# Kernel tuning notes

Hardware: AMD Instinct MI355X
Metric: run time of the kernel (lower is better)

## Reference

```python
import jax, jax.numpy as jnp
import numpy as np

N_NODES = 50000
C = 128
E = 800000
B = 4096
NEG = 5
NUM_LAYERS = 3


def setup_inputs() -> dict:
    key = jax.random.key(0)
    ks = jax.random.split(key, 8)
    edge_index = jax.random.randint(ks[0], (2, E), 0, N_NODES, dtype=jnp.int64)
    edge_weight = jax.random.uniform(ks[1], (E,), dtype=jnp.float32)
    n_id = jax.random.randint(ks[2], ((2 + NEG) * B,), 0, N_NODES, dtype=jnp.int64)
    x = jnp.zeros((1,), jnp.float32)  # ignored by forward (overwritten by id_embed)
    id_embed = jax.random.normal(ks[3], (N_NODES, C), jnp.float32) * 0.1
    w1 = jax.random.normal(ks[4], (2 * C, C), jnp.float32) * (1.0 / np.sqrt(2 * C))
    b1 = jnp.zeros((C,), jnp.float32)
    w2 = jax.random.normal(ks[5], (C, 1), jnp.float32) * (1.0 / np.sqrt(C))
    b2 = jnp.zeros((1,), jnp.float32)
    return {"x": x, "edge_index": edge_index, "edge_weight": edge_weight,
            "n_id": n_id, "neg_sample_num": NEG, "id_embed": id_embed,
            "w1": w1, "b1": b1, "w2": w2, "b2": b2}


def reference(x, edge_index, edge_weight, n_id, neg_sample_num, id_embed, w1, b1, w2, b2):
    n_nodes = id_embed.shape[0]
    row, col = edge_index[0], edge_index[1]
    # symmetric GCN normalization (LGCConv)
    deg = jax.ops.segment_sum(jnp.ones_like(row, dtype=id_embed.dtype), row,
                              num_segments=n_nodes)
    dinv = jnp.where(deg > 0, jax.lax.rsqrt(jnp.maximum(deg, 1e-12)), 0.0)
    norm = (dinv[row] * dinv[col])[:, None]  # [E,1]
    h = id_embed
    final = id_embed
    for _ in range(NUM_LAYERS):
        h = jax.ops.segment_sum(norm * h[col], row, num_segments=n_nodes)
        final = final + h
    final = final / (NUM_LAYERS + 1)
    # split n_id into (out, pos, neg) index groups
    b = n_id.shape[0] // (2 + neg_sample_num)
    out = final[n_id[:b]]
    pos = final[n_id[b:2 * b]]
    neg = final[n_id[2 * b:]]
    tiled_out = jnp.repeat(out, neg_sample_num, axis=0)  # [b*neg, C]

    def pred_head(z):  # Linear -> LeakyReLU(0.2) -> (Dropout eval=identity) -> Linear
        z = jax.nn.leaky_relu(z @ w1 + b1, negative_slope=0.2)
        return z @ w2 + b2

    pos_logit = pred_head(jnp.concatenate([out, pos], axis=-1))
    neg_logits = pred_head(jnp.concatenate([tiled_out, neg], axis=-1))
    return pos_logit, neg_logits
```

## Files before the change

kernel.cpp:

```cpp
#include <hip/hip_runtime.h>
#include <hip/hip_bf16.h>

#define C 128
#define NBKT 128
#define BCAP 8192

typedef __bf16 bf16x8 __attribute__((ext_vector_type(8)));
typedef float floatx4 __attribute__((ext_vector_type(4)));

__device__ __forceinline__ unsigned short f2bf(float f) {
    unsigned u = __float_as_uint(f);
    unsigned r = (u + 0x7FFFu + ((u >> 16) & 1u)) >> 16;
    return (unsigned short)r;
}
__device__ __forceinline__ float bflo(unsigned v) { return __uint_as_float(v << 16); }
__device__ __forceinline__ float bfhi(unsigned v) { return __uint_as_float(v & 0xFFFF0000u); }
__device__ __forceinline__ unsigned packbf(float lo, float hi) {
    return (unsigned)f2bf(lo) | ((unsigned)f2bf(hi) << 16);
}

__device__ __forceinline__ int g_idx(const void* p, long long i, int is64) {
    if (is64) return (int)((const long long*)p)[i];
    return ((const int*)p)[i];
}
__device__ __forceinline__ float g_flt(const void* p, long long i, int isf32) {
    if (isf32) return ((const float*)p)[i];
    return __uint_as_float(((unsigned)((const unsigned short*)p)[i]) << 16);
}

__global__ void k_detect(const void* edge, const void* nid, const void* emb, int* flags,
                         unsigned* g0, unsigned* g1, unsigned* g2, int* bucketcnt,
                         int N, int SST) {
    int t = threadIdx.x;
    int buf = t >> 6, w = t & 63;
    size_t o = (size_t)(w >> 5) * SST + (size_t)N * 32 + (w & 31);
    if (buf == 0) g0[o] = 0;
    else if (buf == 1) g1[o] = 0;
    else g2[o] = 0;
    if (t < NBKT) bucketcnt[t] = 0;
    if (t < 64) {
        const unsigned* wrd = (const unsigned*)edge;
        const unsigned* nw = (const unsigned*)nid;
        int predA = (t < 32) ? (wrd[2 * t + 1] == 0u) : 1;
        int predB = (t < 32) ? (nw[2 * t + 1] == 0u) : 1;
        const unsigned short* h = (const unsigned short*)emb;
        int ex = (h[2 * t] >> 7) & 0xFF;
        int plaus = (ex >= 0x6C && ex <= 0x7F) ? 1 : 0;
        unsigned long long mA = __ballot(predA);
        unsigned long long mB = __ballot(predB);
        unsigned long long mP = __ballot(plaus);
        if (t == 0) {
            flags[0] = (mA == ~0ull) ? 1 : 0;
            flags[1] = (mB == ~0ull) ? 1 : 0;
            flags[2] = (__popcll(mP) < 32) ? 1 : 0;
        }
    }
}

__global__ void k_bucketA(const void* edge, int E, int rpb, const int* flags,
                          unsigned* __restrict__ bucketbuf, int* __restrict__ bucketcnt) {
    __shared__ int lcnt[NBKT];
    __shared__ int lbase[NBKT];
    int t = threadIdx.x;
    int is64 = flags[0];
    const int PER = 8;
    int chunkSz = blockDim.x * PER;
    long long stride = (long long)gridDim.x * chunkSz;
    for (long long base = (long long)blockIdx.x * chunkSz; base < E; base += stride) {
        if (t < NBKT) lcnt[t] = 0;
        __syncthreads();
        int bkt[PER], rank[PER];
        unsigned enc[PER];
        long long e0 = base + (long long)t * PER;
        int rr[PER], cc[PER];
        if (e0 + PER <= E) {
            if (is64) {
                const long long* pr = (const long long*)edge + e0;
                const long long* pc = (const long long*)edge + E + e0;
#pragma unroll
                for (int j = 0; j < PER; j += 2) {
                    longlong2 vr = *(const longlong2*)(pr + j);
                    longlong2 vc = *(const longlong2*)(pc + j);
                    rr[j] = (int)vr.x; rr[j + 1] = (int)vr.y;
                    cc[j] = (int)vc.x; cc[j + 1] = (int)vc.y;
                }
            } else {
                const int* pr = (const int*)edge + e0;
                const int* pc = (const int*)edge + E + e0;
#pragma unroll
                for (int j = 0; j < PER; j += 4) {
                    int4 vr = *(const int4*)(pr + j);
                    int4 vc = *(const int4*)(pc + j);
                    rr[j] = vr.x; rr[j + 1] = vr.y; rr[j + 2] = vr.z; rr[j + 3] = vr.w;
                    cc[j] = vc.x; cc[j + 1] = vc.y; cc[j + 2] = vc.z; cc[j + 3] = vc.w;
                }
            }
#pragma unroll
            for (int j = 0; j < PER; ++j) {
                int b = rr[j] / rpb;
                bkt[j] = b;
                enc[j] = ((unsigned)(rr[j] - b * rpb) << 16) | (unsigned)(cc[j] & 0xFFFF);
                rank[j] = atomicAdd(&lcnt[b], 1);
            }
        } else {
#pragma unroll
            for (int j = 0; j < PER; ++j) {
                long long e = e0 + j;
                if (e < E) {
                    int r = g_idx(edge, e, is64);
                    int c = g_idx(edge, (long long)E + e, is64);
                    int b = r / rpb;
                    bkt[j] = b;
                    enc[j] = ((unsigned)(r - b * rpb) << 16) | (unsigned)(c & 0xFFFF);
                    rank[j] = atomicAdd(&lcnt[b], 1);
                } else bkt[j] = -1;
            }
        }
        __syncthreads();
        if (t < NBKT) lbase[t] = atomicAdd(&bucketcnt[t], lcnt[t]);
        __syncthreads();
#pragma unroll
        for (int j = 0; j < PER; ++j) {
            if (bkt[j] >= 0) {
                int pos = lbase[bkt[j]] + rank[j];
                if (pos < BCAP)
                    bucketbuf[(size_t)bkt[j] * BCAP + pos] = enc[j];
            }
        }
    }
}

__global__ __launch_bounds__(512) void k_bsort(
        const unsigned* __restrict__ bucketbuf, const int* __restrict__ bucketcnt,
        int* __restrict__ rowptr, float* __restrict__ dinv, float* __restrict__ di2,
        float* __restrict__ rdinv, unsigned short* __restrict__ cols16, int N, int rpb) {
    __shared__ int hist[512];
    int b = blockIdx.x;
    int t = threadIdx.x;
    int base = 0, cnt = 0, total = 0;
    for (int i = 0; i < NBKT; ++i) {
        int v = bucketcnt[i];
        if (v > BCAP) v = BCAP;
        if (i < b) base += v;
        if (i == b) cnt = v;
        total += v;
    }
    int r0 = b * rpb;
    int rows = N - r0;
    if (rows > rpb) rows = rpb;
    if (rows < 0) rows = 0;

    hist[t] = 0;
    __syncthreads();
    const unsigned* buf = bucketbuf + (size_t)b * BCAP;
    for (int i = t; i < cnt; i += 512) atomicAdd(&hist[buf[i] >> 16], 1);
    __syncthreads();
    int v = hist[t];
    __syncthreads();
    for (int off = 1; off < 512; off <<= 1) {
        int x = (t >= off) ? hist[t - off] : 0;
        __syncthreads();
        hist[t] += x;
        __syncthreads();
    }
    int excl = hist[t] - v;
    if (t < rows) {
        int r = r0 + t;
        rowptr[r] = base + excl;
        float fd = (float)v;
        float dv = (v > 0) ? rsqrtf(fd) : 0.0f;
        dinv[r] = dv;
        di2[r] = dv * dv;
        rdinv[r] = (v > 0) ? sqrtf(fd) : 0.0f;
    }
    if (b == NBKT - 1 && t == 0) rowptr[N] = total;
    __syncthreads();
    hist[t] = base + excl;
    __syncthreads();
    for (int i = t; i < cnt; i += 512) {
        unsigned u = buf[i];
        int pos = atomicAdd(&hist[u >> 16], 1);
        cols16[pos] = (unsigned short)(u & 0xFFFF);
    }
}

__global__ void k_initprep(const void* emb, const float* __restrict__ dinv,
                           unsigned* __restrict__ h0, unsigned* __restrict__ g0,
                           int n2, int SST,
                           const void* w1, const void* b1, const void* w2, const void* b2,
                           unsigned short* __restrict__ w1t, float* __restrict__ b1f,
                           float* __restrict__ w2f, float* __restrict__ b2f, const int* flags) {
    int i = blockIdx.x * blockDim.x + threadIdx.x;
    int f32 = flags[2];
    if (i < n2) {
        float lo = g_flt(emb, 2LL * i, f32);
        float hi = g_flt(emb, 2LL * i + 1, f32);
        int n = i >> 6, w = i & 63;
        size_t o = (size_t)(w >> 5) * SST + (size_t)n * 32 + (w & 31);
        h0[o] = packbf(lo, hi);
        float dv = dinv[n];
        g0[o] = packbf(lo * dv, hi * dv);
    }
    if (i < 256 * 128) {
        int k = i >> 7, n = i & 127;
        w1t[n * 256 + k] = f2bf(g_flt(w1, i, f32));
    }
    if (i < 128) {
        b1f[i] = g_flt(b1, i, f32);
        w2f[i] = g_flt(w2, i, f32);
    }
    if (i == 0) b2f[0] = g_flt(b2, 0, f32);
}

__global__ void k_layer(const int* __restrict__ rowptr, const unsigned short* __restrict__ cols16,
                        const uint4* __restrict__ gin, uint4* __restrict__ gout,
                        const float* __restrict__ di2, int N, int SSTU4) {
    int slice = blockIdx.x & 1;
    int node = (blockIdx.x >> 1) * 32 + (threadIdx.x >> 3);
    if (node >= N) return;
    int l8 = threadIdx.x & 7;
    const uint4* gs = gin + (size_t)slice * SSTU4;
    int p = rowptr[node];
    int end = rowptr[node + 1];
    float a0 = 0.f, a1 = 0.f, a2 = 0.f, a3 = 0.f;
    float a4 = 0.f, a5 = 0.f, a6 = 0.f, a7 = 0.f;
    for (int base = p; base < end; base += 8) {
        int c[8];
#pragma unroll
        for (int j = 0; j < 8; ++j) {
            int idx = base + j;
            int cv = cols16[idx];
            c[j] = (idx < end) ? cv : N;
        }
#pragma unroll
        for (int j = 0; j < 8; ++j) {
            uint4 v = gs[(size_t)c[j] * 8 + l8];
            a0 += bflo(v.x); a1 += bfhi(v.x);
            a2 += bflo(v.y); a3 += bfhi(v.y);
            a4 += bflo(v.z); a5 += bfhi(v.z);
            a6 += bflo(v.w); a7 += bfhi(v.w);
        }
    }
    float s = di2[node];
    uint4 o;
    o.x = packbf(a0 * s, a1 * s);
    o.y = packbf(a2 * s, a3 * s);
    o.z = packbf(a4 * s, a5 * s);
    o.w = packbf(a6 * s, a7 * s);
    gout[(size_t)slice * SSTU4 + (size_t)node * 8 + l8] = o;
}

__global__ void k_layer3(const int* __restrict__ rowptr, const unsigned short* __restrict__ cols16,
                         const uint4* __restrict__ gin , const uint4* __restrict__ h0,
                         const uint4* __restrict__ g1, uint4* __restrict__ fin,
                         const float* __restrict__ di2, const float* __restrict__ rdinv,
                         int N, int SSTU4) {
    int slice = blockIdx.x & 1;
    int node = (blockIdx.x >> 1) * 32 + (threadIdx.x >> 3);
    if (node >= N) return;
    int l8 = threadIdx.x & 7;
    size_t sb = (size_t)slice * SSTU4;
    const uint4* gs = gin + sb;
    int p = rowptr[node];
    int end = rowptr[node + 1];
    float a0 = 0.f, a1 = 0.f, a2 = 0.f, a3 = 0.f;
    float a4 = 0.f, a5 = 0.f, a6 = 0.f, a7 = 0.f;
    for (int base = p; base < end; base += 8) {
        int c[8];
#pragma unroll
        for (int j = 0; j < 8; ++j) {
            int idx = base + j;
            int cv = cols16[idx];
            c[j] = (idx < end) ? cv : N;
        }
#pragma unroll
        for (int j = 0; j < 8; ++j) {
            uint4 v = gs[(size_t)c[j] * 8 + l8];
            a0 += bflo(v.x); a1 += bfhi(v.x);
            a2 += bflo(v.y); a3 += bfhi(v.y);
            a4 += bflo(v.z); a5 += bfhi(v.z);
            a6 += bflo(v.w); a7 += bfhi(v.w);
        }
    }
    float s = di2[node];
    float rd = rdinv[node];
    size_t ro = (size_t)node * 8 + l8;
    uint4 x0 = h0[sb + ro];
    uint4 x1 = g1[sb + ro];
    uint4 x2 = gs[ro];
    uint4 o;
    o.x = packbf(0.25f * (bflo(x0.x) + rd * (bflo(x1.x) + bflo(x2.x) + s * a0)),
                 0.25f * (bfhi(x0.x) + rd * (bfhi(x1.x) + bfhi(x2.x) + s * a1)));
    o.y = packbf(0.25f * (bflo(x0.y) + rd * (bflo(x1.y) + bflo(x2.y) + s * a2)),
                 0.25f * (bfhi(x0.y) + rd * (bfhi(x1.y) + bfhi(x2.y) + s * a3)));
    o.z = packbf(0.25f * (bflo(x0.z) + rd * (bflo(x1.z) + bflo(x2.z) + s * a4)),
                 0.25f * (bfhi(x0.z) + rd * (bfhi(x1.z) + bfhi(x2.z) + s * a5)));
    o.w = packbf(0.25f * (bflo(x0.w) + rd * (bflo(x1.w) + bflo(x2.w) + s * a6)),
                 0.25f * (bfhi(x0.w) + rd * (bfhi(x1.w) + bfhi(x2.w) + s * a7)));
    fin[(size_t)node * 16 + slice * 8 + l8] = o;
}

__global__ void k_head(const uint4* __restrict__ fin, const void* n_id,
                       const unsigned short* __restrict__ w1t,
                       const float* __restrict__ b1f, const float* __restrict__ w2f,
                       const float* __restrict__ b2f,
                       float* __restrict__ out, int B, int NEG, const int* flags) {
    __shared__ unsigned short z[64][264];
    int t = threadIdx.x;
    int id64 = flags[1];
    int mbase = blockIdx.x * 64;

#pragma unroll
    for (int i = 0; i < 8; ++i) {
        int flat = i * 256 + t;
        int m = flat >> 5;
        int q = flat & 31;
        int gm = mbase + m;
        int r;
        if (gm < B) {
            r = (q < 16) ? g_idx(n_id, gm, id64) : g_idx(n_id, B + gm, id64);
        } else {
            int j = gm - B;
            r = (q < 16) ? g_idx(n_id, j / NEG, id64) : g_idx(n_id, 2 * B + j, id64);
        }
        uint4 v = fin[(size_t)r * 16 + (q & 15)];
        *(uint4*)((char*)&z[m][0] + q * 16) = v;
    }
    __syncthreads();

    int wave = t >> 6, lane = t & 63;
    int quad = lane >> 4, l16 = lane & 15;

    floatx4 acc[8] = {};
    bf16x8 a[8];
    const unsigned short* zrow = &z[wave * 16 + l16][0];
#pragma unroll
    for (int ks = 0; ks < 8; ++ks)
        a[ks] = *(const bf16x8*)(zrow + ks * 32 + quad * 8);

#pragma unroll
    for (int ks = 0; ks < 8; ++ks) {
#pragma unroll
        for (int nt = 0; nt < 8; ++nt) {
            bf16x8 b = *(const bf16x8*)(w1t + (nt * 16 + l16) * 256 + ks * 32 + quad * 8);
            acc[nt] = __builtin_amdgcn_mfma_f32_16x16x32_bf16(a[ks], b, acc[nt], 0, 0, 0);
        }
    }

    float s0 = 0.f, s1 = 0.f, s2 = 0.f, s3 = 0.f;
#pragma unroll
    for (int nt = 0; nt < 8; ++nt) {
        int col = nt * 16 + l16;
        float bb = b1f[col], ww = w2f[col];
        float v0 = acc[nt][0] + bb; v0 = (v0 > 0.f) ? v0 : 0.2f * v0; s0 += v0 * ww;
        float v1 = acc[nt][1] + bb; v1 = (v1 > 0.f) ? v1 : 0.2f * v1; s1 += v1 * ww;
        float v2 = acc[nt][2] + bb; v2 = (v2 > 0.f) ? v2 : 0.2f * v2; s2 += v2 * ww;
        float v3 = acc[nt][3] + bb; v3 = (v3 > 0.f) ? v3 : 0.2f * v3; s3 += v3 * ww;
    }
#pragma unroll
    for (int off = 1; off <= 8; off <<= 1) {
        s0 += __shfl_xor(s0, off, 64);
        s1 += __shfl_xor(s1, off, 64);
        s2 += __shfl_xor(s2, off, 64);
        s3 += __shfl_xor(s3, off, 64);
    }
    if (l16 == 0) {
        int rowbase = mbase + wave * 16 + quad * 4;
        float bb2 = b2f[0];
        out[rowbase + 0] = s0 + bb2;
        out[rowbase + 1] = s1 + bb2;
        out[rowbase + 2] = s2 + bb2;
        out[rowbase + 3] = s3 + bb2;
    }
}

extern "C" void kernel_launch(void* const* d_in, const int* in_sizes, int n_in,
                              void* d_out, int out_size, void* d_ws, size_t ws_size,
                              hipStream_t stream) {
    const void* edge_index = d_in[1];
    const void* n_id       = d_in[3];
    const void* id_embed   = d_in[5];
    const void* w1 = d_in[6];
    const void* b1 = d_in[7];
    const void* w2 = d_in[8];
    const void* b2 = d_in[9];
    float* out = (float*)d_out;

    const int E  = in_sizes[1] / 2;
    const int N  = in_sizes[5] / C;
    const int NEG = 5;
    const int B  = in_sizes[3] / (2 + NEG);
    const int n_out_rows = B + B * NEG;
    const int SST = (N + 1) * 32;
    const int SSTU4 = (N + 1) * 8;
    const int NB = 2 * SST;
    const int rpb = (N + NBKT - 1) / NBKT;

    size_t off = 0;
    auto alloc = [&](size_t nf) {
        char* p = (char*)d_ws + off * 4;
        off += (nf + 255) & ~(size_t)255;
        return p;
    };
    int*   flags     = (int*)alloc(8);
    int*   bucketcnt = (int*)alloc(NBKT);
    float* dinv      = (float*)alloc(N);
    float* di2       = (float*)alloc(N);
    float* rdinv     = (float*)alloc(N);
    int*   rowptr    = (int*)alloc(N + 1);
    unsigned short* cols16 = (unsigned short*)alloc(((size_t)E + 16 + 1) / 2);
    unsigned* bucketbuf = (unsigned*)alloc((size_t)NBKT * BCAP);
    unsigned* h0     = (unsigned*)alloc(NB);
    unsigned* g0     = (unsigned*)alloc(NB);
    unsigned* g1     = (unsigned*)alloc(NB);
    unsigned* g2     = (unsigned*)alloc(NB);
    unsigned* fin    = (unsigned*)alloc((size_t)N * 64);
    unsigned short* w1t = (unsigned short*)alloc(256 * 128 / 2);
    float* b1f       = (float*)alloc(C);
    float* w2f       = (float*)alloc(C);
    float* b2f       = (float*)alloc(8);

    const int BS = 256;
    k_detect<<<1, 192, 0, stream>>>(edge_index, n_id, id_embed, flags, g0, g1, g2,
                                    bucketcnt, N, SST);
    const int gridA = (E + BS * 8 - 1) / (BS * 8);
    k_bucketA<<<gridA, BS, 0, stream>>>(edge_index, E, rpb, flags, bucketbuf, bucketcnt);
    k_bsort<<<NBKT, 512, 0, stream>>>(bucketbuf, bucketcnt, rowptr, dinv, di2, rdinv,
                                      cols16, N, rpb);
    k_initprep<<<(N * 64 + BS - 1) / BS, BS, 0, stream>>>(
        id_embed, dinv, h0, g0, N * 64, SST, w1, b1, w2, b2, w1t, b1f, w2f, b2f, flags);

    const int layer_grid = ((N + 31) / 32) * 2;
    k_layer<<<layer_grid, BS, 0, stream>>>(rowptr, cols16, (const uint4*)g0, (uint4*)g1,
                                           di2, N, SSTU4);
    k_layer<<<layer_grid, BS, 0, stream>>>(rowptr, cols16, (const uint4*)g1, (uint4*)g2,
                                           di2, N, SSTU4);
    k_layer3<<<layer_grid, BS, 0, stream>>>(rowptr, cols16, (const uint4*)g2, (const uint4*)h0,
                                            (const uint4*)g1, (uint4*)fin, di2, rdinv,
                                            N, SSTU4);

    k_head<<<n_out_rows / 64, BS, 0, stream>>>((const uint4*)fin, n_id, w1t, b1f, w2f, b2f,
                                               out, B, NEG, flags);
}
```

Baseline: 216.0 us.

## Split node features into four 32-channel slices for SpMM gather locality

Feature buffers are re-laid out from two 64-channel slices into four 32-channel slices (64 bytes per node per slice). Each layer kernel now assigns 4 lanes per node, 64 nodes per block, and interleaves block indices so that pairs of tiles run on the same slice. The aim is to shrink each slice's working set so gathered rows stay resident in cache, and to read the column indices with nontemporal loads so they do not evict feature data. The cost is that each edge's column index is reread four times instead of twice, and each gather touches only 64 bytes.

```diff
diff --git a/kernel.cpp b/kernel.cpp
--- a/kernel.cpp
+++ b/kernel.cpp
@@ -33,7 +33,7 @@
                          int N, int SST) {
     int t = threadIdx.x;
     int buf = t >> 6, w = t & 63;
-    size_t o = (size_t)(w >> 5) * SST + (size_t)N * 32 + (w & 31);
+    size_t o = (size_t)(w >> 4) * SST + (size_t)N * 16 + (w & 15);
     if (buf == 0) g0[o] = 0;
     else if (buf == 1) g1[o] = 0;
     else g2[o] = 0;
@@ -186,39 +186,48 @@
 
 __global__ void k_initprep(const void* emb, const float* __restrict__ dinv,
                            unsigned* __restrict__ h0, unsigned* __restrict__ g0,
-                           int n2, int SST,
+                           int N, int SST,
                            const void* w1, const void* b1, const void* w2, const void* b2,
                            unsigned short* __restrict__ w1t, float* __restrict__ b1f,
                            float* __restrict__ w2f, float* __restrict__ b2f, const int* flags) {
-    int i = blockIdx.x * blockDim.x + threadIdx.x;
+    int t = threadIdx.x;
+    int b = blockIdx.x;
     int f32 = flags[2];
-    if (i < n2) {
-        float lo = g_flt(emb, 2LL * i, f32);
-        float hi = g_flt(emb, 2LL * i + 1, f32);
-        int n = i >> 6, w = i & 63;
-        size_t o = (size_t)(w >> 5) * SST + (size_t)n * 32 + (w & 31);
+    int s = (b & 7) >> 1;
+    int local = ((b >> 3) << 1) | (b & 1);
+    int k = local * 256 + t;
+    if (k < N * 16) {
+        int n = k >> 4;
+        int within = k & 15;
+        int w = s * 16 + within;
+        float lo = g_flt(emb, (long long)n * 128 + 2 * w, f32);
+        float hi = g_flt(emb, (long long)n * 128 + 2 * w + 1, f32);
+        size_t o = (size_t)s * SST + (size_t)n * 16 + within;
         h0[o] = packbf(lo, hi);
         float dv = dinv[n];
         g0[o] = packbf(lo * dv, hi * dv);
     }
-    if (i < 256 * 128) {
-        int k = i >> 7, n = i & 127;
-        w1t[n * 256 + k] = f2bf(g_flt(w1, i, f32));
-    }
-    if (i < 128) {
-        b1f[i] = g_flt(b1, i, f32);
-        w2f[i] = g_flt(w2, i, f32);
-    }
-    if (i == 0) b2f[0] = g_flt(b2, 0, f32);
+    int flat = b * 256 + t;
+    if (flat < 256 * 128) {
+        int kk = flat >> 7, n = flat & 127;
+        w1t[n * 256 + kk] = f2bf(g_flt(w1, flat, f32));
+    }
+    if (flat < 128) {
+        b1f[flat] = g_flt(b1, flat, f32);
+        w2f[flat] = g_flt(w2, flat, f32);
+    }
+    if (flat == 0) b2f[0] = g_flt(b2, 0, f32);
 }
 
 __global__ void k_layer(const int* __restrict__ rowptr, const unsigned short* __restrict__ cols16,
                         const uint4* __restrict__ gin, uint4* __restrict__ gout,
                         const float* __restrict__ di2, int N, int SSTU4) {
-    int slice = blockIdx.x & 1;
-    int node = (blockIdx.x >> 1) * 32 + (threadIdx.x >> 3);
+    int b = blockIdx.x;
+    int slice = (b & 7) >> 1;
+    int tile = ((b >> 3) << 1) | (b & 1);
+    int node = tile * 64 + (threadIdx.x >> 2);
     if (node >= N) return;
-    int l8 = threadIdx.x & 7;
+    int l4 = threadIdx.x & 3;
     const uint4* gs = gin + (size_t)slice * SSTU4;
     int p = rowptr[node];
     int end = rowptr[node + 1];
@@ -229,12 +238,12 @@
 #pragma unroll
         for (int j = 0; j < 8; ++j) {
             int idx = base + j;
-            int cv = cols16[idx];
+            int cv = __builtin_nontemporal_load(cols16 + idx);
             c[j] = (idx < end) ? cv : N;
         }
 #pragma unroll
         for (int j = 0; j < 8; ++j) {
-            uint4 v = gs[(size_t)c[j] * 8 + l8];
+            uint4 v = gs[(size_t)c[j] * 4 + l4];
             a0 += bflo(v.x); a1 += bfhi(v.x);
             a2 += bflo(v.y); a3 += bfhi(v.y);
             a4 += bflo(v.z); a5 += bfhi(v.z);
@@ -247,7 +256,7 @@
     o.y = packbf(a2 * s, a3 * s);
     o.z = packbf(a4 * s, a5 * s);
     o.w = packbf(a6 * s, a7 * s);
-    gout[(size_t)slice * SSTU4 + (size_t)node * 8 + l8] = o;
+    gout[(size_t)slice * SSTU4 + (size_t)node * 4 + l4] = o;
 }
 
 __global__ void k_layer3(const int* __restrict__ rowptr, const unsigned short* __restrict__ cols16,
@@ -255,10 +264,12 @@
                          const uint4* __restrict__ g1, uint4* __restrict__ fin,
                          const float* __restrict__ di2, const float* __restrict__ rdinv,
                          int N, int SSTU4) {
-    int slice = blockIdx.x & 1;
-    int node = (blockIdx.x >> 1) * 32 + (threadIdx.x >> 3);
+    int b = blockIdx.x;
+    int slice = (b & 7) >> 1;
+    int tile = ((b >> 3) << 1) | (b & 1);
+    int node = tile * 64 + (threadIdx.x >> 2);
     if (node >= N) return;
-    int l8 = threadIdx.x & 7;
+    int l4 = threadIdx.x & 3;
     size_t sb = (size_t)slice * SSTU4;
     const uint4* gs = gin + sb;
     int p = rowptr[node];
@@ -270,12 +281,12 @@
 #pragma unroll
         for (int j = 0; j < 8; ++j) {
             int idx = base + j;
-            int cv = cols16[idx];
+            int cv = __builtin_nontemporal_load(cols16 + idx);
             c[j] = (idx < end) ? cv : N;
         }
 #pragma unroll
         for (int j = 0; j < 8; ++j) {
-            uint4 v = gs[(size_t)c[j] * 8 + l8];
+            uint4 v = gs[(size_t)c[j] * 4 + l4];
             a0 += bflo(v.x); a1 += bfhi(v.x);
             a2 += bflo(v.y); a3 += bfhi(v.y);
             a4 += bflo(v.z); a5 += bfhi(v.z);
@@ -284,7 +295,7 @@
     }
     float s = di2[node];
     float rd = rdinv[node];
-    size_t ro = (size_t)node * 8 + l8;
+    size_t ro = (size_t)node * 4 + l4;
     uint4 x0 = h0[sb + ro];
     uint4 x1 = g1[sb + ro];
     uint4 x2 = gs[ro];
@@ -297,7 +308,7 @@
                  0.25f * (bfhi(x0.z) + rd * (bfhi(x1.z) + bfhi(x2.z) + s * a5)));
     o.w = packbf(0.25f * (bflo(x0.w) + rd * (bflo(x1.w) + bflo(x2.w) + s * a6)),
                  0.25f * (bfhi(x0.w) + rd * (bfhi(x1.w) + bfhi(x2.w) + s * a7)));
-    fin[(size_t)node * 16 + slice * 8 + l8] = o;
+    fin[(size_t)node * 16 + slice * 4 + l4] = o;
 }
 
 __global__ void k_head(const uint4* __restrict__ fin, const void* n_id,
@@ -391,9 +402,9 @@
     const int NEG = 5;
     const int B  = in_sizes[3] / (2 + NEG);
     const int n_out_rows = B + B * NEG;
-    const int SST = (N + 1) * 32;
-    const int SSTU4 = (N + 1) * 8;
-    const int NB = 2 * SST;
+    const int SST = (N + 1) * 16;
+    const int SSTU4 = (N + 1) * 4;
+    const int NB = 4 * SST;
     const int rpb = (N + NBKT - 1) / NBKT;
 
     size_t off = 0;
@@ -427,10 +438,14 @@
     k_bucketA<<<gridA, BS, 0, stream>>>(edge_index, E, rpb, flags, bucketbuf, bucketcnt);
     k_bsort<<<NBKT, 512, 0, stream>>>(bucketbuf, bucketcnt, rowptr, dinv, di2, rdinv,
                                       cols16, N, rpb);
-    k_initprep<<<(N * 64 + BS - 1) / BS, BS, 0, stream>>>(
-        id_embed, dinv, h0, g0, N * 64, SST, w1, b1, w2, b2, w1t, b1f, w2f, b2f, flags);
-
-    const int layer_grid = ((N + 31) / 32) * 2;
+
+    const int nbi = (N * 16 + BS - 1) / BS;
+    const int igrid = ((nbi + 1) / 2) * 8;
+    k_initprep<<<igrid, BS, 0, stream>>>(
+        id_embed, dinv, h0, g0, N, SST, w1, b1, w2, b2, w1t, b1f, w2f, b2f, flags);
+
+    const int tiles = (N + 63) / 64;
+    const int layer_grid = ((tiles + 1) / 2) * 8;
     k_layer<<<layer_grid, BS, 0, stream>>>(rowptr, cols16, (const uint4*)g0, (uint4*)g1,
                                            di2, N, SSTU4);
     k_layer<<<layer_grid, BS, 0, stream>>>(rowptr, cols16, (const uint4*)g1, (uint4*)g2,
```

New measurement: 248.6 us. +15.1%, slower.

## Replace bucket sort CSR build with atomic count/scatter and half-split padded rows

Applied to the files above, without the earlier changes.

Replaces the two-pass bucket sort with a global atomic degree count, a per-block partial sum plus scan, and an atomic scatter into a CSR whose rows are split into two halves by column index and padded to multiples of eight with a dummy node. The layer kernels then load eight column indices per vector load with no bounds masking, and process the low-column half before the high-column half with a block barrier in between, aiming for better cache locality in the gathers. This adds more kernel launches, padding entries and global atomics on a large cursor array, and the scatter order inside a row becomes nondeterministic.

```diff
diff --git a/kernel.cpp b/kernel.cpp
--- a/kernel.cpp
+++ b/kernel.cpp
@@ -3,10 +3,10 @@
 
 #define C 128
 #define NBKT 128
-#define BCAP 8192
 
 typedef __bf16 bf16x8 __attribute__((ext_vector_type(8)));
 typedef float floatx4 __attribute__((ext_vector_type(4)));
+typedef unsigned short u16x8 __attribute__((ext_vector_type(8)));
 
 __device__ __forceinline__ unsigned short f2bf(float f) {
     unsigned u = __float_as_uint(f);
@@ -29,133 +29,133 @@
 }
 
 __global__ void k_detect(const void* edge, const void* nid, const void* emb, int* flags,
-                         unsigned* g0, unsigned* g1, unsigned* g2, int* bucketcnt,
-                         int N, int SST) {
-    int t = threadIdx.x;
-    int buf = t >> 6, w = t & 63;
-    size_t o = (size_t)(w >> 5) * SST + (size_t)N * 32 + (w & 31);
-    if (buf == 0) g0[o] = 0;
-    else if (buf == 1) g1[o] = 0;
-    else g2[o] = 0;
-    if (t < NBKT) bucketcnt[t] = 0;
-    if (t < 64) {
-        const unsigned* wrd = (const unsigned*)edge;
-        const unsigned* nw = (const unsigned*)nid;
-        int predA = (t < 32) ? (wrd[2 * t + 1] == 0u) : 1;
-        int predB = (t < 32) ? (nw[2 * t + 1] == 0u) : 1;
-        const unsigned short* h = (const unsigned short*)emb;
-        int ex = (h[2 * t] >> 7) & 0xFF;
-        int plaus = (ex >= 0x6C && ex <= 0x7F) ? 1 : 0;
-        unsigned long long mA = __ballot(predA);
-        unsigned long long mB = __ballot(predB);
-        unsigned long long mP = __ballot(plaus);
-        if (t == 0) {
-            flags[0] = (mA == ~0ull) ? 1 : 0;
-            flags[1] = (mB == ~0ull) ? 1 : 0;
-            flags[2] = (__popcll(mP) < 32) ? 1 : 0;
-        }
-    }
-}
-
-__global__ void k_bucketA(const void* edge, int E, int rpb, const int* flags,
-                          unsigned* __restrict__ bucketbuf, int* __restrict__ bucketcnt) {
-    __shared__ int lcnt[NBKT];
-    __shared__ int lbase[NBKT];
-    int t = threadIdx.x;
+                         unsigned* h0, unsigned* g0, unsigned* g1, unsigned* g2,
+                         int* deg2, int twoN, int N, int SST) {
+    int gid = blockIdx.x * blockDim.x + threadIdx.x;
+    for (int i = gid; i < twoN; i += gridDim.x * blockDim.x) deg2[i] = 0;
+    if (blockIdx.x == 0) {
+        int t = threadIdx.x;
+        int buf = t >> 6, w = t & 63;
+        size_t o = (size_t)(w >> 5) * SST + (size_t)N * 32 + (w & 31);
+        if (buf == 0) g0[o] = 0;
+        else if (buf == 1) g1[o] = 0;
+        else if (buf == 2) g2[o] = 0;
+        else h0[o] = 0;
+        if (t < 64) {
+            const unsigned* wrd = (const unsigned*)edge;
+            const unsigned* nw = (const unsigned*)nid;
+            int predA = (t < 32) ? (wrd[2 * t + 1] == 0u) : 1;
+            int predB = (t < 32) ? (nw[2 * t + 1] == 0u) : 1;
+            const unsigned short* h = (const unsigned short*)emb;
+            int ex = (h[2 * t] >> 7) & 0xFF;
+            int plaus = (ex >= 0x6C && ex <= 0x7F) ? 1 : 0;
+            unsigned long long mA = __ballot(predA);
+            unsigned long long mB = __ballot(predB);
+            unsigned long long mP = __ballot(plaus);
+            if (t == 0) {
+                flags[0] = (mA == ~0ull) ? 1 : 0;
+                flags[1] = (mB == ~0ull) ? 1 : 0;
+                flags[2] = (__popcll(mP) < 32) ? 1 : 0;
+            }
+        }
+    }
+}
+
+__global__ void k_count(const void* edge, int E, int Nhalf, const int* flags,
+                        int* __restrict__ deg2) {
     int is64 = flags[0];
     const int PER = 8;
-    int chunkSz = blockDim.x * PER;
-    long long stride = (long long)gridDim.x * chunkSz;
-    for (long long base = (long long)blockIdx.x * chunkSz; base < E; base += stride) {
-        if (t < NBKT) lcnt[t] = 0;
-        __syncthreads();
-        int bkt[PER], rank[PER];
-        unsigned enc[PER];
-        long long e0 = base + (long long)t * PER;
-        int rr[PER], cc[PER];
-        if (e0 + PER <= E) {
-            if (is64) {
-                const long long* pr = (const long long*)edge + e0;
-                const long long* pc = (const long long*)edge + E + e0;
-#pragma unroll
-                for (int j = 0; j < PER; j += 2) {
-                    longlong2 vr = *(const longlong2*)(pr + j);
-                    longlong2 vc = *(const longlong2*)(pc + j);
-                    rr[j] = (int)vr.x; rr[j + 1] = (int)vr.y;
-                    cc[j] = (int)vc.x; cc[j + 1] = (int)vc.y;
-                }
-            } else {
-                const int* pr = (const int*)edge + e0;
-                const int* pc = (const int*)edge + E + e0;
-#pragma unroll
-                for (int j = 0; j < PER; j += 4) {
-                    int4 vr = *(const int4*)(pr + j);
-                    int4 vc = *(const int4*)(pc + j);
-                    rr[j] = vr.x; rr[j + 1] = vr.y; rr[j + 2] = vr.z; rr[j + 3] = vr.w;
-                    cc[j] = vc.x; cc[j + 1] = vc.y; cc[j + 2] = vc.z; cc[j + 3] = vc.w;
-                }
-            }
-#pragma unroll
-            for (int j = 0; j < PER; ++j) {
-                int b = rr[j] / rpb;
-                bkt[j] = b;
-                enc[j] = ((unsigned)(rr[j] - b * rpb) << 16) | (unsigned)(cc[j] & 0xFFFF);
-                rank[j] = atomicAdd(&lcnt[b], 1);
+    int t = threadIdx.x;
+    long long e0 = ((long long)blockIdx.x * blockDim.x + t) * PER;
+    int rr[PER], cc[PER];
+    if (e0 + PER <= E) {
+        if (is64) {
+            const long long* pr = (const long long*)edge + e0;
+            const long long* pc = (const long long*)edge + E + e0;
+#pragma unroll
+            for (int j = 0; j < PER; j += 2) {
+                longlong2 vr = *(const longlong2*)(pr + j);
+                longlong2 vc = *(const longlong2*)(pc + j);
+                rr[j] = (int)vr.x; rr[j + 1] = (int)vr.y;
+                cc[j] = (int)vc.x; cc[j + 1] = (int)vc.y;
             }
         } else {
-#pragma unroll
-            for (int j = 0; j < PER; ++j) {
-                long long e = e0 + j;
-                if (e < E) {
-                    int r = g_idx(edge, e, is64);
-                    int c = g_idx(edge, (long long)E + e, is64);
-                    int b = r / rpb;
-                    bkt[j] = b;
-                    enc[j] = ((unsigned)(r - b * rpb) << 16) | (unsigned)(c & 0xFFFF);
-                    rank[j] = atomicAdd(&lcnt[b], 1);
-                } else bkt[j] = -1;
-            }
-        }
-        __syncthreads();
-        if (t < NBKT) lbase[t] = atomicAdd(&bucketcnt[t], lcnt[t]);
-        __syncthreads();
+            const int* pr = (const int*)edge + e0;
+            const int* pc = (const int*)edge + E + e0;
+#pragma unroll
+            for (int j = 0; j < PER; j += 4) {
+                int4 vr = *(const int4*)(pr + j);
+                int4 vc = *(const int4*)(pc + j);
+                rr[j] = vr.x; rr[j + 1] = vr.y; rr[j + 2] = vr.z; rr[j + 3] = vr.w;
+                cc[j] = vc.x; cc[j + 1] = vc.y; cc[j + 2] = vc.z; cc[j + 3] = vc.w;
+            }
+        }
+#pragma unroll
+        for (int j = 0; j < PER; ++j)
+            atomicAdd(&deg2[2 * rr[j] + (cc[j] >= Nhalf)], 1);
+    } else {
 #pragma unroll
         for (int j = 0; j < PER; ++j) {
-            if (bkt[j] >= 0) {
-                int pos = lbase[bkt[j]] + rank[j];
-                if (pos < BCAP)
-                    bucketbuf[(size_t)bkt[j] * BCAP + pos] = enc[j];
-            }
-        }
-    }
-}
-
-__global__ __launch_bounds__(512) void k_bsort(
-        const unsigned* __restrict__ bucketbuf, const int* __restrict__ bucketcnt,
-        int* __restrict__ rowptr, float* __restrict__ dinv, float* __restrict__ di2,
-        float* __restrict__ rdinv, unsigned short* __restrict__ cols16, int N, int rpb) {
-    __shared__ int hist[512];
-    int b = blockIdx.x;
-    int t = threadIdx.x;
-    int base = 0, cnt = 0, total = 0;
-    for (int i = 0; i < NBKT; ++i) {
-        int v = bucketcnt[i];
-        if (v > BCAP) v = BCAP;
-        if (i < b) base += v;
-        if (i == b) cnt = v;
-        total += v;
-    }
+            long long e = e0 + j;
+            if (e < E) {
+                int r = g_idx(edge, e, is64);
+                int c = g_idx(edge, (long long)E + e, is64);
+                atomicAdd(&deg2[2 * r + (c >= Nhalf)], 1);
+            }
+        }
+    }
+}
+
+__global__ __launch_bounds__(256) void k_pbsum(const int* __restrict__ deg2,
+                                               int* __restrict__ pbsum, int N, int rpb) {
+    __shared__ int red[256];
+    int b = blockIdx.x, t = threadIdx.x;
     int r0 = b * rpb;
     int rows = N - r0;
     if (rows > rpb) rows = rpb;
     if (rows < 0) rows = 0;
-
-    hist[t] = 0;
+    int s = 0;
+    for (int i = t; i < rows; i += 256) {
+        int d0 = deg2[2 * (r0 + i)];
+        int d1 = deg2[2 * (r0 + i) + 1];
+        s += ((d0 + 7) & ~7) + ((d1 + 7) & ~7);
+    }
+    red[t] = s;
     __syncthreads();
-    const unsigned* buf = bucketbuf + (size_t)b * BCAP;
-    for (int i = t; i < cnt; i += 512) atomicAdd(&hist[buf[i] >> 16], 1);
-    __syncthreads();
-    int v = hist[t];
+    for (int o = 128; o > 0; o >>= 1) {
+        if (t < o) red[t] += red[t + o];
+        __syncthreads();
+    }
+    if (t == 0) pbsum[b] = red[0];
+}
+
+__global__ __launch_bounds__(512) void k_scan(
+        const int* __restrict__ deg2, const int* __restrict__ pbsum,
+        int* __restrict__ rowptrA, int* __restrict__ tcnt, int* __restrict__ cursor,
+        unsigned short* __restrict__ cols16,
+        float* __restrict__ dinv, float* __restrict__ di2, float* __restrict__ rdinv,
+        int N, int rpb) {
+    __shared__ int hist[512];
+    __shared__ int sbase;
+    int b = blockIdx.x, t = threadIdx.x;
+    if (t == 0) {
+        int s = 0;
+        for (int i = 0; i < b; ++i) s += pbsum[i];
+        sbase = s;
+    }
+    int r0 = b * rpb;
+    int rows = N - r0;
+    if (rows > rpb) rows = rpb;
+    if (rows < 0) rows = 0;
+    int d0 = 0, d1 = 0, p0 = 0, p1 = 0, p = 0;
+    if (t < rows) {
+        d0 = deg2[2 * (r0 + t)];
+        d1 = deg2[2 * (r0 + t) + 1];
+        p0 = (d0 + 7) & ~7;
+        p1 = (d1 + 7) & ~7;
+        p = p0 + p1;
+    }
+    hist[t] = p;
     __syncthreads();
     for (int off = 1; off < 512; off <<= 1) {
         int x = (t >= off) ? hist[t - off] : 0;
@@ -163,24 +163,76 @@
         hist[t] += x;
         __syncthreads();
     }
-    int excl = hist[t] - v;
+    int start = sbase + hist[t] - p;
     if (t < rows) {
         int r = r0 + t;
-        rowptr[r] = base + excl;
-        float fd = (float)v;
-        float dv = (v > 0) ? rsqrtf(fd) : 0.0f;
+        rowptrA[r] = start;
+        cursor[2 * r] = start;
+        cursor[2 * r + 1] = start + p0;
+        tcnt[r] = (p0 >> 3) | ((p1 >> 3) << 16);
+        int d = d0 + d1;
+        float fd = (float)d;
+        float dv = (d > 0) ? rsqrtf(fd) : 0.0f;
         dinv[r] = dv;
         di2[r] = dv * dv;
-        rdinv[r] = (v > 0) ? sqrtf(fd) : 0.0f;
-    }
-    if (b == NBKT - 1 && t == 0) rowptr[N] = total;
-    __syncthreads();
-    hist[t] = base + excl;
-    __syncthreads();
-    for (int i = t; i < cnt; i += 512) {
-        unsigned u = buf[i];
-        int pos = atomicAdd(&hist[u >> 16], 1);
-        cols16[pos] = (unsigned short)(u & 0xFFFF);
+        rdinv[r] = (d > 0) ? sqrtf(fd) : 0.0f;
+        for (int k = d0; k < p0; ++k) cols16[start + k] = (unsigned short)N;
+        for (int k = d1; k < p1; ++k) cols16[start + p0 + k] = (unsigned short)N;
+    }
+    if (b == NBKT - 1 && t == 0) {
+        rowptrA[N] = sbase + hist[511];
+        tcnt[N] = 0;
+        dinv[N] = 0.f; di2[N] = 0.f; rdinv[N] = 0.f;
+    }
+}
+
+__global__ void k_scatter(const void* edge, int E, int Nhalf, const int* flags,
+                          int* __restrict__ cursor, unsigned short* __restrict__ cols16) {
+    int is64 = flags[0];
+    const int PER = 8;
+    int t = threadIdx.x;
+    long long e0 = ((long long)blockIdx.x * blockDim.x + t) * PER;
+    int rr[PER], cc[PER];
+    if (e0 + PER <= E) {
+        if (is64) {
+            const long long* pr = (const long long*)edge + e0;
+            const long long* pc = (const long long*)edge + E + e0;
+#pragma unroll
+            for (int j = 0; j < PER; j += 2) {
+                longlong2 vr = *(const longlong2*)(pr + j);
+                longlong2 vc = *(const longlong2*)(pc + j);
+                rr[j] = (int)vr.x; rr[j + 1] = (int)vr.y;
+                cc[j] = (int)vc.x; cc[j + 1] = (int)vc.y;
+            }
+        } else {
+            const int* pr = (const int*)edge + e0;
+            const int* pc = (const int*)edge + E + e0;
+#pragma unroll
+            for (int j = 0; j < PER; j += 4) {
+                int4 vr = *(const int4*)(pr + j);
+                int4 vc = *(const int4*)(pc + j);
+                rr[j] = vr.x; rr[j + 1] = vr.y; rr[j + 2] = vr.z; rr[j + 3] = vr.w;
+                cc[j] = vc.x; cc[j + 1] = vc.y; cc[j + 2] = vc.z; cc[j + 3] = vc.w;
+            }
+        }
+#pragma unroll
+        for (int j = 0; j < PER; ++j) {
+            int h = (cc[j] >= Nhalf);
+            int pos = atomicAdd(&cursor[2 * rr[j] + h], 1);
+            cols16[pos] = (unsigned short)cc[j];
+        }
+    } else {
+#pragma unroll
+        for (int j = 0; j < PER; ++j) {
+            long long e = e0 + j;
+            if (e < E) {
+                int r = g_idx(edge, e, is64);
+                int c = g_idx(edge, (long long)E + e, is64);
+                int h = (c >= Nhalf);
+                int pos = atomicAdd(&cursor[2 * r + h], 1);
+                cols16[pos] = (unsigned short)c;
+            }
+        }
     }
 }
 
@@ -212,29 +264,38 @@
     if (i == 0) b2f[0] = g_flt(b2, 0, f32);
 }
 
-__global__ void k_layer(const int* __restrict__ rowptr, const unsigned short* __restrict__ cols16,
+__global__ void k_layer(const int* __restrict__ rowptrA, const int* __restrict__ tcnt,
+                        const unsigned short* __restrict__ cols16,
                         const uint4* __restrict__ gin, uint4* __restrict__ gout,
                         const float* __restrict__ di2, int N, int SSTU4) {
-    int slice = blockIdx.x & 1;
-    int node = (blockIdx.x >> 1) * 32 + (threadIdx.x >> 3);
-    if (node >= N) return;
+    int b = blockIdx.x;
+    int slice = b & 1;
+    int node = (b >> 1) * 32 + (threadIdx.x >> 3);
+    if (node > N) node = N;
     int l8 = threadIdx.x & 7;
     const uint4* gs = gin + (size_t)slice * SSTU4;
-    int p = rowptr[node];
-    int end = rowptr[node + 1];
+    int base = rowptrA[node];
+    int tc = tcnt[node];
+    int t0 = tc & 0xFFFF, t1 = (tc >> 16) & 0xFFFF;
     float a0 = 0.f, a1 = 0.f, a2 = 0.f, a3 = 0.f;
     float a4 = 0.f, a5 = 0.f, a6 = 0.f, a7 = 0.f;
-    for (int base = p; base < end; base += 8) {
-        int c[8];
+    for (int i = 0; i < t0; ++i, base += 8) {
+        u16x8 cv = *(const u16x8*)(cols16 + base);
 #pragma unroll
         for (int j = 0; j < 8; ++j) {
-            int idx = base + j;
-            int cv = cols16[idx];
-            c[j] = (idx < end) ? cv : N;
-        }
+            uint4 v = gs[(size_t)cv[j] * 8 + l8];
+            a0 += bflo(v.x); a1 += bfhi(v.x);
+            a2 += bflo(v.y); a3 += bfhi(v.y);
+            a4 += bflo(v.z); a5 += bfhi(v.z);
+            a6 += bflo(v.w); a7 += bfhi(v.w);
+        }
+    }
+    __syncthreads();
+    for (int i = 0; i < t1; ++i, base += 8) {
+        u16x8 cv = *(const u16x8*)(cols16 + base);
 #pragma unroll
         for (int j = 0; j < 8; ++j) {
-            uint4 v = gs[(size_t)c[j] * 8 + l8];
+            uint4 v = gs[(size_t)cv[j] * 8 + l8];
             a0 += bflo(v.x); a1 += bfhi(v.x);
             a2 += bflo(v.y); a3 += bfhi(v.y);
             a4 += bflo(v.z); a5 += bfhi(v.z);
@@ -250,32 +311,41 @@
     gout[(size_t)slice * SSTU4 + (size_t)node * 8 + l8] = o;
 }
 
-__global__ void k_layer3(const int* __restrict__ rowptr, const unsigned short* __restrict__ cols16,
+__global__ void k_layer3(const int* __restrict__ rowptrA, const int* __restrict__ tcnt,
+                         const unsigned short* __restrict__ cols16,
                          const uint4* __restrict__ gin , const uint4* __restrict__ h0,
                          const uint4* __restrict__ g1, uint4* __restrict__ fin,
                          const float* __restrict__ di2, const float* __restrict__ rdinv,
                          int N, int SSTU4) {
-    int slice = blockIdx.x & 1;
-    int node = (blockIdx.x >> 1) * 32 + (threadIdx.x >> 3);
-    if (node >= N) return;
+    int b = blockIdx.x;
+    int slice = b & 1;
+    int node = (b >> 1) * 32 + (threadIdx.x >> 3);
+    if (node > N) node = N;
     int l8 = threadIdx.x & 7;
     size_t sb = (size_t)slice * SSTU4;
     const uint4* gs = gin + sb;
-    int p = rowptr[node];
-    int end = rowptr[node + 1];
+    int base = rowptrA[node];
+    int tc = tcnt[node];
+    int t0 = tc & 0xFFFF, t1 = (tc >> 16) & 0xFFFF;
     float a0 = 0.f, a1 = 0.f, a2 = 0.f, a3 = 0.f;
     float a4 = 0.f, a5 = 0.f, a6 = 0.f, a7 = 0.f;
-    for (int base = p; base < end; base += 8) {
-        int c[8];
+    for (int i = 0; i < t0; ++i, base += 8) {
+        u16x8 cv = *(const u16x8*)(cols16 + base);
 #pragma unroll
         for (int j = 0; j < 8; ++j) {
-            int idx = base + j;
-            int cv = cols16[idx];
-            c[j] = (idx < end) ? cv : N;
-        }
+            uint4 v = gs[(size_t)cv[j] * 8 + l8];
+            a0 += bflo(v.x); a1 += bfhi(v.x);
+            a2 += bflo(v.y); a3 += bfhi(v.y);
+            a4 += bflo(v.z); a5 += bfhi(v.z);
+            a6 += bflo(v.w); a7 += bfhi(v.w);
+        }
+    }
+    __syncthreads();
+    for (int i = 0; i < t1; ++i, base += 8) {
+        u16x8 cv = *(const u16x8*)(cols16 + base);
 #pragma unroll
         for (int j = 0; j < 8; ++j) {
-            uint4 v = gs[(size_t)c[j] * 8 + l8];
+            uint4 v = gs[(size_t)cv[j] * 8 + l8];
             a0 += bflo(v.x); a1 += bfhi(v.x);
             a2 += bflo(v.y); a3 += bfhi(v.y);
             a4 += bflo(v.z); a5 += bfhi(v.z);
@@ -395,6 +465,7 @@
     const int SSTU4 = (N + 1) * 8;
     const int NB = 2 * SST;
     const int rpb = (N + NBKT - 1) / NBKT;
+    const int Nhalf = N / 2;
 
     size_t off = 0;
     auto alloc = [&](size_t nf) {
@@ -403,41 +474,46 @@
         return p;
     };
     int*   flags     = (int*)alloc(8);
-    int*   bucketcnt = (int*)alloc(NBKT);
-    float* dinv      = (float*)alloc(N);
-    float* di2       = (float*)alloc(N);
-    float* rdinv     = (float*)alloc(N);
-    int*   rowptr    = (int*)alloc(N + 1);
-    unsigned short* cols16 = (unsigned short*)alloc(((size_t)E + 16 + 1) / 2);
-    unsigned* bucketbuf = (unsigned*)alloc((size_t)NBKT * BCAP);
+    int*   deg2      = (int*)alloc(2 * (size_t)N);
+    int*   pbsum     = (int*)alloc(NBKT);
+    int*   cursor    = (int*)alloc(2 * (size_t)N);
+    float* dinv      = (float*)alloc(N + 1);
+    float* di2       = (float*)alloc(N + 1);
+    float* rdinv     = (float*)alloc(N + 1);
+    int*   rowptrA   = (int*)alloc(N + 1);
+    int*   tcnt      = (int*)alloc(N + 1);
+    unsigned short* cols16 = (unsigned short*)alloc(((size_t)E + 16 * (size_t)N) / 2 + 8);
     unsigned* h0     = (unsigned*)alloc(NB);
     unsigned* g0     = (unsigned*)alloc(NB);
     unsigned* g1     = (unsigned*)alloc(NB);
     unsigned* g2     = (unsigned*)alloc(NB);
-    unsigned* fin    = (unsigned*)alloc((size_t)N * 64);
+    unsigned* fin    = (unsigned*)alloc((size_t)(N + 1) * 64);
     unsigned short* w1t = (unsigned short*)alloc(256 * 128 / 2);
     float* b1f       = (float*)alloc(C);
     float* w2f       = (float*)alloc(C);
     float* b2f       = (float*)alloc(8);
 
     const int BS = 256;
-    k_detect<<<1, 192, 0, stream>>>(edge_index, n_id, id_embed, flags, g0, g1, g2,
-                                    bucketcnt, N, SST);
-    const int gridA = (E + BS * 8 - 1) / (BS * 8);
-    k_bucketA<<<gridA, BS, 0, stream>>>(edge_index, E, rpb, flags, bucketbuf, bucketcnt);
-    k_bsort<<<NBKT, 512, 0, stream>>>(bucketbuf, bucketcnt, rowptr, dinv, di2, rdinv,
-                                      cols16, N, rpb);
+    k_detect<<<128, BS, 0, stream>>>(edge_index, n_id, id_embed, flags, h0, g0, g1, g2,
+                                     deg2, 2 * N, N, SST);
+    const int gridE = (E + BS * 8 - 1) / (BS * 8);
+    k_count<<<gridE, BS, 0, stream>>>(edge_index, E, Nhalf, flags, deg2);
+    k_pbsum<<<NBKT, BS, 0, stream>>>(deg2, pbsum, N, rpb);
+    k_scan<<<NBKT, 512, 0, stream>>>(deg2, pbsum, rowptrA, tcnt, cursor, cols16,
+                                     dinv, di2, rdinv, N, rpb);
+    k_scatter<<<gridE, BS, 0, stream>>>(edge_index, E, Nhalf, flags, cursor, cols16);
+
     k_initprep<<<(N * 64 + BS - 1) / BS, BS, 0, stream>>>(
         id_embed, dinv, h0, g0, N * 64, SST, w1, b1, w2, b2, w1t, b1f, w2f, b2f, flags);
 
     const int layer_grid = ((N + 31) / 32) * 2;
-    k_layer<<<layer_grid, BS, 0, stream>>>(rowptr, cols16, (const uint4*)g0, (uint4*)g1,
-                                           di2, N, SSTU4);
-    k_layer<<<layer_grid, BS, 0, stream>>>(rowptr, cols16, (const uint4*)g1, (uint4*)g2,
-                                           di2, N, SSTU4);
-    k_layer3<<<layer_grid, BS, 0, stream>>>(rowptr, cols16, (const uint4*)g2, (const uint4*)h0,
-                                            (const uint4*)g1, (uint4*)fin, di2, rdinv,
-                                            N, SSTU4);
+    k_layer<<<layer_grid, BS, 0, stream>>>(rowptrA, tcnt, cols16, (const uint4*)g0,
+                                           (uint4*)g1, di2, N, SSTU4);
+    k_layer<<<layer_grid, BS, 0, stream>>>(rowptrA, tcnt, cols16, (const uint4*)g1,
+                                           (uint4*)g2, di2, N, SSTU4);
+    k_layer3<<<layer_grid, BS, 0, stream>>>(rowptrA, tcnt, cols16, (const uint4*)g2,
+                                            (const uint4*)h0, (const uint4*)g1, (uint4*)fin,
+                                            di2, rdinv, N, SSTU4);
 
     k_head<<<n_out_rows / 64, BS, 0, stream>>>((const uint4*)fin, n_id, w1t, b1f, w2f, b2f,
                                                out, B, NEG, flags);
```

After: 283.7 us. 1.31x slower.
